# Kernel optimization log

Measured on AMD Instinct MI355X. Metric: run time of the kernel, lower is better.

The kernel has to match this reference:

```python
import jax, jax.numpy as jnp
import numpy as np

SEQ, BATCH, IN, HID, OUT = 512, 64, 64, 1024, 1


def _lstm_layer(x, W_ih, W_hh, b_ih, b_hh):
    # x: [T, B, I]; PyTorch gate order: i, f, g, o along 4H axis
    B = x.shape[1]
    H = W_hh.shape[1]
    xg = jnp.einsum('tbi,gi->tbg', x, W_ih) + b_ih + b_hh  # [T, B, 4H]

    def step(carry, xg_t):
        h, c = carry
        gates = xg_t + h @ W_hh.T  # [B, 4H]
        i, f, g, o = jnp.split(gates, 4, axis=-1)
        i = jax.nn.sigmoid(i)
        f = jax.nn.sigmoid(f)
        g = jnp.tanh(g)
        o = jax.nn.sigmoid(o)
        c = f * c + i * g
        h = o * jnp.tanh(c)
        return (h, c), h

    h0 = jnp.zeros((B, H), x.dtype)
    (_, _), hs = jax.lax.scan(step, (h0, h0), xg)
    return hs  # [T, B, H]


def setup_inputs() -> dict:
    key = jax.random.key(0)
    ks = jax.random.split(key, 12)
    s0 = 1.0 / np.sqrt(HID)
    d = {
        'x': jax.random.normal(ks[0], (SEQ, BATCH, IN), jnp.float32),
        'W_ih0': jax.random.uniform(ks[1], (4 * HID, IN), jnp.float32, -s0, s0),
        'W_hh0': jax.random.uniform(ks[2], (4 * HID, HID), jnp.float32, -s0, s0),
        'b_ih0': jax.random.uniform(ks[3], (4 * HID,), jnp.float32, -s0, s0),
        'b_hh0': jax.random.uniform(ks[4], (4 * HID,), jnp.float32, -s0, s0),
        'W_ih1': jax.random.uniform(ks[5], (4 * HID, HID), jnp.float32, -s0, s0),
        'W_hh1': jax.random.uniform(ks[6], (4 * HID, HID), jnp.float32, -s0, s0),
        'b_ih1': jax.random.uniform(ks[7], (4 * HID,), jnp.float32, -s0, s0),
        'b_hh1': jax.random.uniform(ks[8], (4 * HID,), jnp.float32, -s0, s0),
        'W_lin': jax.random.uniform(ks[9], (OUT, HID), jnp.float32, -s0, s0),
        'b_lin': jax.random.uniform(ks[10], (OUT,), jnp.float32, -s0, s0),
    }
    return d


def reference(x, W_ih0, W_hh0, b_ih0, b_hh0, W_ih1, W_hh1, b_ih1, b_hh1, W_lin, b_lin):
    h1 = _lstm_layer(x, W_ih0, W_hh0, b_ih0, b_hh0)   # [T, B, H]
    lstm_out = _lstm_layer(h1, W_ih1, W_hh1, b_ih1, b_hh1)  # [T, B, H]
    y_pred = lstm_out[-1] @ W_lin.T + b_lin           # [B, 1]
    return lstm_out, y_pred.reshape(-1)
```

## Files before the change

kernel.cpp:

```cpp
#include <hip/hip_runtime.h>
#include <stdint.h>

#define SEQ   512
#define BATCH 64
#define INP   64
#define HID   1024
#define NBLK  512
#define NTHR  256
#define CHK   32
#define NCH   (HID / CHK)
#define PRE   (CHK * 64 / NTHR)

__device__ __forceinline__ float cload(float* p) {
    return __hip_atomic_load(p, __ATOMIC_RELAXED, __HIP_MEMORY_SCOPE_AGENT);
}
__device__ __forceinline__ void cstore(float* p, float v) {
    __hip_atomic_store(p, v, __ATOMIC_RELAXED, __HIP_MEMORY_SCOPE_AGENT);
}

__device__ __forceinline__ float sigf(float x) { return 1.0f / (1.0f + __expf(-x)); }

__device__ __forceinline__ void flagbar(uint32_t* flags, int tid) {
    __syncthreads();
    if (tid == 0)
        __hip_atomic_store(&flags[blockIdx.x], 1u, __ATOMIC_RELAXED, __HIP_MEMORY_SCOPE_AGENT);
    if (tid < 64) {
        for (;;) {
            bool ok = true;
            #pragma unroll
            for (int i = 0; i < NBLK / 64; ++i) {
                uint32_t v = __hip_atomic_load(&flags[tid + i * 64], __ATOMIC_RELAXED,
                                               __HIP_MEMORY_SCOPE_AGENT);
                ok &= ((uint32_t)(v - 1u) < 0x10000000u);
            }
            if (__all(ok)) break;
        }
    }
    __syncthreads();
}

__device__ __forceinline__ void bar_arrive(uint32_t* grp, int tid) {
    __syncthreads();
    if (tid == 0)
        __hip_atomic_fetch_add(&grp[blockIdx.x & 7], 1u, __ATOMIC_RELAXED,
                               __HIP_MEMORY_SCOPE_AGENT);
}
__device__ __forceinline__ void bar_wait(uint32_t* grp, uint32_t target, int tid) {
    if (tid < 64) {
        for (;;) {
            uint32_t v = __hip_atomic_load(&grp[tid & 7], __ATOMIC_RELAXED,
                                           __HIP_MEMORY_SCOPE_AGENT);
            if (__all((uint32_t)(v - target) < 0x10000000u)) break;
        }
    }
    __syncthreads();
}

__global__ void __launch_bounds__(NTHR, 2) lstm_fused(
    const float* __restrict__ x,
    const float* __restrict__ Wih0, const float* __restrict__ Whh0,
    const float* __restrict__ bih0, const float* __restrict__ bhh0,
    const float* __restrict__ Wih1, const float* __restrict__ Whh1,
    const float* __restrict__ bih1, const float* __restrict__ bhh1,
    float* __restrict__ out, float* __restrict__ h0buf, float* __restrict__ h2buf,
    uint32_t* __restrict__ flags, uint32_t* __restrict__ grp)
{
    __shared__ float Wsh[4][HID][4];
    __shared__ float st1[CHK * 64];
    __shared__ float st2[CHK * 64];
    const int tid = threadIdx.x;
    const int bk  = blockIdx.x;
    const bool Lb = (bk >= NBLK / 2);
    const int ub  = (Lb ? bk - NBLK / 2 : bk) * 4;
    const int u   = tid >> 6;
    const int b   = tid & 63;
    const int j   = ub + u;
    const int js  = ub + __builtin_amdgcn_readfirstlane(u);

    const float* Whh = Lb ? Whh1 : Whh0;
    for (int idx = tid; idx < 4 * 4 * HID; idx += NTHR) {
        int uu = idx >> 12, g = (idx >> 10) & 3, k = idx & (HID - 1);
        Wsh[uu][k][g] = Whh[((size_t)(g * HID + ub + uu)) * HID + k];
    }
    const float* bi = Lb ? bih1 : bih0;
    const float* bh = Lb ? bhh1 : bhh0;
    const float bias0 = bi[0 * HID + j] + bh[0 * HID + j];
    const float bias1 = bi[1 * HID + j] + bh[1 * HID + j];
    const float bias2 = bi[2 * HID + j] + bh[2 * HID + j];
    const float bias3 = bi[3 * HID + j] + bh[3 * HID + j];

    cstore((Lb ? h2buf : h0buf) + j * 64 + b, 0.0f);
    if (bk < 8 && tid == 0) {
        __hip_atomic_store(&grp[bk], 0u, __ATOMIC_RELAXED, __HIP_MEMORY_SCOPE_AGENT);
        __threadfence();
    }
    float c = 0.0f;
    flagbar(flags, tid);

    if (!Lb) {
        const float4* wi0 = (const float4*)(Wih0 + (size_t)(0 * HID + js) * INP);
        const float4* wi1 = (const float4*)(Wih0 + (size_t)(1 * HID + js) * INP);
        const float4* wi2 = (const float4*)(Wih0 + (size_t)(2 * HID + js) * INP);
        const float4* wi3 = (const float4*)(Wih0 + (size_t)(3 * HID + js) * INP);
        float a0 = bias0, a1 = bias1, a2 = bias2, a3 = bias3;
        {
            const float4* xr = (const float4*)(x + (size_t)b * INP);
            #pragma unroll
            for (int k4 = 0; k4 < INP / 4; ++k4) {
                float4 xv = xr[k4];
                float4 u0 = wi0[k4], u1 = wi1[k4], u2 = wi2[k4], u3 = wi3[k4];
                a0 += u0.x * xv.x + u0.y * xv.y + u0.z * xv.z + u0.w * xv.w;
                a1 += u1.x * xv.x + u1.y * xv.y + u1.z * xv.z + u1.w * xv.w;
                a2 += u2.x * xv.x + u2.y * xv.y + u2.z * xv.z + u2.w * xv.w;
                a3 += u3.x * xv.x + u3.y * xv.y + u3.z * xv.z + u3.w * xv.w;
            }
        }
        for (int t = 0; t < SEQ; ++t) {
            float* hr = h0buf + (t & 1) * (HID * 64);
            float* hw = h0buf + ((t & 1) ^ 1) * (HID * 64);
            float pre[PRE];
            #pragma unroll
            for (int i = 0; i < PRE; ++i) pre[i] = cload(hr + i * NTHR + tid);
            for (int cc = 0; cc < NCH; ++cc) {
                __syncthreads();
                #pragma unroll
                for (int i = 0; i < PRE; ++i) st1[i * NTHR + tid] = pre[i];
                if (cc + 1 < NCH) {
                    float* src = hr + (cc + 1) * (CHK * 64);
                    #pragma unroll
                    for (int i = 0; i < PRE; ++i) pre[i] = cload(src + i * NTHR + tid);
                }
                __syncthreads();
                #pragma unroll
                for (int kk = 0; kk < CHK; ++kk) {
                    int k = cc * CHK + kk;
                    float  hv = st1[kk * 64 + b];
                    float4 w  = *(const float4*)&Wsh[u][k][0];
                    a0 += w.x * hv; a1 += w.y * hv; a2 += w.z * hv; a3 += w.w * hv;
                }
            }
            float ig = sigf(a0), fg = sigf(a1), gg = tanhf(a2), og = sigf(a3);
            c = fg * c + ig * gg;
            float h = og * tanhf(c);
            cstore(hw + j * 64 + b, h);
            bar_arrive(grp, tid);
            if (t + 1 < SEQ) {
                a0 = bias0; a1 = bias1; a2 = bias2; a3 = bias3;
                const float4* xr = (const float4*)(x + ((size_t)(t + 1) * BATCH + b) * INP);
                #pragma unroll
                for (int k4 = 0; k4 < INP / 4; ++k4) {
                    float4 xv = xr[k4];
                    float4 u0 = wi0[k4], u1 = wi1[k4], u2 = wi2[k4], u3 = wi3[k4];
                    a0 += u0.x * xv.x + u0.y * xv.y + u0.z * xv.z + u0.w * xv.w;
                    a1 += u1.x * xv.x + u1.y * xv.y + u1.z * xv.z + u1.w * xv.w;
                    a2 += u2.x * xv.x + u2.y * xv.y + u2.z * xv.z + u2.w * xv.w;
                    a3 += u3.x * xv.x + u3.y * xv.y + u3.z * xv.z + u3.w * xv.w;
                }
                bar_wait(grp, (uint32_t)(t + 1) * 64u, tid);
            }
        }
    } else {
        const float* wr0 = Wih1 + (size_t)(0 * HID + js) * HID;
        const float* wr1 = Wih1 + (size_t)(1 * HID + js) * HID;
        const float* wr2 = Wih1 + (size_t)(2 * HID + js) * HID;
        const float* wr3 = Wih1 + (size_t)(3 * HID + js) * HID;
        for (int t = 0; t < SEQ; ++t) {
            bar_arrive(grp, tid);
            bar_wait(grp, (uint32_t)(t + 1) * 64u, tid);
            float* h1r = h0buf + ((t & 1) ^ 1) * (HID * 64);
            float* h2r = h2buf + (t & 1) * (HID * 64);
            float* h2w = h2buf + ((t & 1) ^ 1) * (HID * 64);
            float a0 = bias0, a1 = bias1, a2 = bias2, a3 = bias3;
            float p1[PRE], p2[PRE];
            #pragma unroll
            for (int i = 0; i < PRE; ++i) p1[i] = cload(h1r + i * NTHR + tid);
            #pragma unroll
            for (int i = 0; i < PRE; ++i) p2[i] = cload(h2r + i * NTHR + tid);
            for (int cc = 0; cc < NCH; ++cc) {
                __syncthreads();
                #pragma unroll
                for (int i = 0; i < PRE; ++i) st1[i * NTHR + tid] = p1[i];
                #pragma unroll
                for (int i = 0; i < PRE; ++i) st2[i * NTHR + tid] = p2[i];
                if (cc + 1 < NCH) {
                    float* s1 = h1r + (cc + 1) * (CHK * 64);
                    float* s2 = h2r + (cc + 1) * (CHK * 64);
                    #pragma unroll
                    for (int i = 0; i < PRE; ++i) p1[i] = cload(s1 + i * NTHR + tid);
                    #pragma unroll
                    for (int i = 0; i < PRE; ++i) p2[i] = cload(s2 + i * NTHR + tid);
                }
                __syncthreads();
                #pragma unroll
                for (int kk = 0; kk < CHK; ++kk) {
                    int k = cc * CHK + kk;
                    float  x1 = st1[kk * 64 + b];
                    float  hv = st2[kk * 64 + b];
                    float4 wh = *(const float4*)&Wsh[u][k][0];
                    a0 += wh.x * hv + wr0[k] * x1;
                    a1 += wh.y * hv + wr1[k] * x1;
                    a2 += wh.z * hv + wr2[k] * x1;
                    a3 += wh.w * hv + wr3[k] * x1;
                }
            }
            float ig = sigf(a0), fg = sigf(a1), gg = tanhf(a2), og = sigf(a3);
            c = fg * c + ig * gg;
            float h = og * tanhf(c);
            cstore(h2w + j * 64 + b, h);
            out[((size_t)t * BATCH + b) * HID + j] = h;
        }
    }
}

__global__ void lstm_finalize(const float* __restrict__ Wlin, const float* __restrict__ blin,
                              float* __restrict__ out, float* __restrict__ h2buf)
{
    __shared__ float red[256];
    const int b = blockIdx.x, tid = threadIdx.x;
    float p = 0.0f;
    for (int k = tid; k < HID; k += 256) p += cload(h2buf + k * 64 + b) * Wlin[k];
    red[tid] = p;
    __syncthreads();
    for (int s = 128; s > 0; s >>= 1) {
        if (tid < s) red[tid] += red[tid + s];
        __syncthreads();
    }
    if (tid == 0) out[(size_t)SEQ * BATCH * HID + b] = blin[0] + red[0];
}

extern "C" void kernel_launch(void* const* d_in, const int* in_sizes, int n_in,
                              void* d_out, int out_size, void* d_ws, size_t ws_size,
                              hipStream_t stream) {
    const float* x     = (const float*)d_in[0];
    const float* Wih0  = (const float*)d_in[1];
    const float* Whh0  = (const float*)d_in[2];
    const float* bih0  = (const float*)d_in[3];
    const float* bhh0  = (const float*)d_in[4];
    const float* Wih1  = (const float*)d_in[5];
    const float* Whh1  = (const float*)d_in[6];
    const float* bih1  = (const float*)d_in[7];
    const float* bhh1  = (const float*)d_in[8];
    const float* Wlin  = (const float*)d_in[9];
    const float* blin  = (const float*)d_in[10];
    float* out = (float*)d_out;

    float* ws = (float*)d_ws;
    float* h0buf = ws;
    float* h2buf = ws + 2 * HID * BATCH;
    uint32_t* flags = (uint32_t*)(ws + 4 * HID * BATCH);
    uint32_t* grp   = flags + NBLK;

    lstm_fused<<<dim3(NBLK), dim3(NTHR), 0, stream>>>(
        x, Wih0, Whh0, bih0, bhh0, Wih1, Whh1, bih1, bhh1, out, h0buf, h2buf, flags, grp);
    lstm_finalize<<<dim3(BATCH), dim3(256), 0, stream>>>(Wlin, blin, out, h2buf);
}
```

Measured before the change: 45.01 ms.

## Double-buffer hidden-state chunk loads with inline-asm dwordx4 coherent loads

```diff
diff --git a/kernel.cpp b/kernel.cpp
--- a/kernel.cpp
+++ b/kernel.cpp
@@ -9,7 +9,15 @@
 #define NTHR  256
 #define CHK   32
 #define NCH   (HID / CHK)
-#define PRE   (CHK * 64 / NTHR)
+
+typedef float f4 __attribute__((ext_vector_type(4)));
+
+__device__ __forceinline__ void cload4(f4* dst, const float* p) {
+    asm volatile("global_load_dwordx4 %0, %1, off sc0 sc1"
+                 : "=&v"(*dst) : "v"(p) : "memory");
+}
+#define WAITVM(n) do { asm volatile("s_waitcnt vmcnt(" #n ")" ::: "memory"); \
+                       __builtin_amdgcn_sched_barrier(0); } while (0)
 
 __device__ __forceinline__ float cload(float* p) {
     return __hip_atomic_load(p, __ATOMIC_RELAXED, __HIP_MEMORY_SCOPE_AGENT);
@@ -118,22 +126,40 @@
         for (int t = 0; t < SEQ; ++t) {
             float* hr = h0buf + (t & 1) * (HID * 64);
             float* hw = h0buf + ((t & 1) ^ 1) * (HID * 64);
-            float pre[PRE];
-            #pragma unroll
-            for (int i = 0; i < PRE; ++i) pre[i] = cload(hr + i * NTHR + tid);
-            for (int cc = 0; cc < NCH; ++cc) {
-                __syncthreads();
-                #pragma unroll
-                for (int i = 0; i < PRE; ++i) st1[i * NTHR + tid] = pre[i];
-                if (cc + 1 < NCH) {
-                    float* src = hr + (cc + 1) * (CHK * 64);
-                    #pragma unroll
-                    for (int i = 0; i < PRE; ++i) pre[i] = cload(src + i * NTHR + tid);
+            f4 pA[2], pB[2];
+            cload4(&pA[0], hr + 0 * 2048 +    0 + tid * 4);
+            cload4(&pA[1], hr + 0 * 2048 + 1024 + tid * 4);
+            cload4(&pB[0], hr + 1 * 2048 +    0 + tid * 4);
+            cload4(&pB[1], hr + 1 * 2048 + 1024 + tid * 4);
+            for (int cc = 0; cc < NCH; cc += 2) {
+                __syncthreads();
+                WAITVM(2);
+                *(f4*)&st1[   0 + tid * 4] = pA[0];
+                *(f4*)&st1[1024 + tid * 4] = pA[1];
+                if (cc + 2 < NCH) {
+                    cload4(&pA[0], hr + (cc + 2) * 2048 +    0 + tid * 4);
+                    cload4(&pA[1], hr + (cc + 2) * 2048 + 1024 + tid * 4);
                 }
                 __syncthreads();
                 #pragma unroll
                 for (int kk = 0; kk < CHK; ++kk) {
                     int k = cc * CHK + kk;
+                    float  hv = st1[kk * 64 + b];
+                    float4 w  = *(const float4*)&Wsh[u][k][0];
+                    a0 += w.x * hv; a1 += w.y * hv; a2 += w.z * hv; a3 += w.w * hv;
+                }
+                __syncthreads();
+                if (cc + 2 < NCH) { WAITVM(2); } else { WAITVM(0); }
+                *(f4*)&st1[   0 + tid * 4] = pB[0];
+                *(f4*)&st1[1024 + tid * 4] = pB[1];
+                if (cc + 3 < NCH) {
+                    cload4(&pB[0], hr + (cc + 3) * 2048 +    0 + tid * 4);
+                    cload4(&pB[1], hr + (cc + 3) * 2048 + 1024 + tid * 4);
+                }
+                __syncthreads();
+                #pragma unroll
+                for (int kk = 0; kk < CHK; ++kk) {
+                    int k = (cc + 1) * CHK + kk;
                     float  hv = st1[kk * 64 + b];
                     float4 w  = *(const float4*)&Wsh[u][k][0];
                     a0 += w.x * hv; a1 += w.y * hv; a2 += w.z * hv; a3 += w.w * hv;
@@ -171,29 +197,52 @@
             float* h2r = h2buf + (t & 1) * (HID * 64);
             float* h2w = h2buf + ((t & 1) ^ 1) * (HID * 64);
             float a0 = bias0, a1 = bias1, a2 = bias2, a3 = bias3;
-            float p1[PRE], p2[PRE];
-            #pragma unroll
-            for (int i = 0; i < PRE; ++i) p1[i] = cload(h1r + i * NTHR + tid);
-            #pragma unroll
-            for (int i = 0; i < PRE; ++i) p2[i] = cload(h2r + i * NTHR + tid);
-            for (int cc = 0; cc < NCH; ++cc) {
-                __syncthreads();
-                #pragma unroll
-                for (int i = 0; i < PRE; ++i) st1[i * NTHR + tid] = p1[i];
-                #pragma unroll
-                for (int i = 0; i < PRE; ++i) st2[i * NTHR + tid] = p2[i];
-                if (cc + 1 < NCH) {
-                    float* s1 = h1r + (cc + 1) * (CHK * 64);
-                    float* s2 = h2r + (cc + 1) * (CHK * 64);
-                    #pragma unroll
-                    for (int i = 0; i < PRE; ++i) p1[i] = cload(s1 + i * NTHR + tid);
-                    #pragma unroll
-                    for (int i = 0; i < PRE; ++i) p2[i] = cload(s2 + i * NTHR + tid);
+            f4 p1A[2], p1B[2], p2A[2], p2B[2];
+            cload4(&p1A[0], h1r +    0 + tid * 4);  cload4(&p1A[1], h1r + 1024 + tid * 4);
+            cload4(&p2A[0], h2r +    0 + tid * 4);  cload4(&p2A[1], h2r + 1024 + tid * 4);
+            cload4(&p1B[0], h1r + 2048 + tid * 4);  cload4(&p1B[1], h1r + 3072 + tid * 4);
+            cload4(&p2B[0], h2r + 2048 + tid * 4);  cload4(&p2B[1], h2r + 3072 + tid * 4);
+            for (int cc = 0; cc < NCH; cc += 2) {
+                __syncthreads();
+                WAITVM(4);
+                *(f4*)&st1[   0 + tid * 4] = p1A[0];
+                *(f4*)&st1[1024 + tid * 4] = p1A[1];
+                *(f4*)&st2[   0 + tid * 4] = p2A[0];
+                *(f4*)&st2[1024 + tid * 4] = p2A[1];
+                if (cc + 2 < NCH) {
+                    const float* s1 = h1r + (cc + 2) * 2048;
+                    const float* s2 = h2r + (cc + 2) * 2048;
+                    cload4(&p1A[0], s1 +    0 + tid * 4);  cload4(&p1A[1], s1 + 1024 + tid * 4);
+                    cload4(&p2A[0], s2 +    0 + tid * 4);  cload4(&p2A[1], s2 + 1024 + tid * 4);
                 }
                 __syncthreads();
                 #pragma unroll
                 for (int kk = 0; kk < CHK; ++kk) {
                     int k = cc * CHK + kk;
+                    float  x1 = st1[kk * 64 + b];
+                    float  hv = st2[kk * 64 + b];
+                    float4 wh = *(const float4*)&Wsh[u][k][0];
+                    a0 += wh.x * hv + wr0[k] * x1;
+                    a1 += wh.y * hv + wr1[k] * x1;
+                    a2 += wh.z * hv + wr2[k] * x1;
+                    a3 += wh.w * hv + wr3[k] * x1;
+                }
+                __syncthreads();
+                if (cc + 2 < NCH) { WAITVM(4); } else { WAITVM(0); }
+                *(f4*)&st1[   0 + tid * 4] = p1B[0];
+                *(f4*)&st1[1024 + tid * 4] = p1B[1];
+                *(f4*)&st2[   0 + tid * 4] = p2B[0];
+                *(f4*)&st2[1024 + tid * 4] = p2B[1];
+                if (cc + 3 < NCH) {
+                    const float* s1 = h1r + (cc + 3) * 2048;
+                    const float* s2 = h2r + (cc + 3) * 2048;
+                    cload4(&p1B[0], s1 +    0 + tid * 4);  cload4(&p1B[1], s1 + 1024 + tid * 4);
+                    cload4(&p2B[0], s2 +    0 + tid * 4);  cload4(&p2B[1], s2 + 1024 + tid * 4);
+                }
+                __syncthreads();
+                #pragma unroll
+                for (int kk = 0; kk < CHK; ++kk) {
+                    int k = (cc + 1) * CHK + kk;
                     float  x1 = st1[kk * 64 + b];
                     float  hv = st2[kk * 64 + b];
                     float4 wh = *(const float4*)&Wsh[u][k][0];
```

Result: slower. 48.33 ms (+7.4%).

## Restructure persistent LSTM: 256 blocks of 8 units, k-interleaved h layout, double-buffered loads

Applied to the files above, without the earlier changes.

```diff
diff --git a/kernel.cpp b/kernel.cpp
--- a/kernel.cpp
+++ b/kernel.cpp
@@ -5,11 +5,28 @@
 #define BATCH 64
 #define INP   64
 #define HID   1024
-#define NBLK  512
-#define NTHR  256
+#define NBLK  256
+#define NTHR  512
+#define NU    8
 #define CHK   32
-#define NCH   (HID / CHK)
-#define PRE   (CHK * 64 / NTHR)
+#define KG    8
+#define NCH   32
+#define CHW   2048
+#define HBUF  65536
+
+typedef float f4 __attribute__((ext_vector_type(4)));
+
+__device__ __forceinline__ void cload4(f4* dst, const float* p) {
+    asm volatile("global_load_dwordx4 %0, %1, off sc0 sc1"
+                 : "=&v"(*dst) : "v"(p) : "memory");
+}
+#define WAITVM(n) do { asm volatile("s_waitcnt vmcnt(" #n ")" ::: "memory"); \
+                       __builtin_amdgcn_sched_barrier(0); } while (0)
+#define BARR  do { __builtin_amdgcn_sched_barrier(0); \
+                   asm volatile("s_waitcnt lgkmcnt(0)" ::: "memory"); \
+                   __builtin_amdgcn_sched_barrier(0); \
+                   __builtin_amdgcn_s_barrier(); \
+                   __builtin_amdgcn_sched_barrier(0); } while (0)
 
 __device__ __forceinline__ float cload(float* p) {
     return __hip_atomic_load(p, __ATOMIC_RELAXED, __HIP_MEMORY_SCOPE_AGENT);
@@ -17,7 +34,6 @@
 __device__ __forceinline__ void cstore(float* p, float v) {
     __hip_atomic_store(p, v, __ATOMIC_RELAXED, __HIP_MEMORY_SCOPE_AGENT);
 }
-
 __device__ __forceinline__ float sigf(float x) { return 1.0f / (1.0f + __expf(-x)); }
 
 __device__ __forceinline__ void flagbar(uint32_t* flags, int tid) {
@@ -56,40 +72,33 @@
     __syncthreads();
 }
 
+
 __global__ void __launch_bounds__(NTHR, 2) lstm_fused(
     const float* __restrict__ x,
     const float* __restrict__ Wih0, const float* __restrict__ Whh0,
     const float* __restrict__ bih0, const float* __restrict__ bhh0,
     const float* __restrict__ Wih1, const float* __restrict__ Whh1,
     const float* __restrict__ bih1, const float* __restrict__ bhh1,
-    float* __restrict__ out, float* __restrict__ h0buf, float* __restrict__ h2buf,
+    float* __restrict__ out, float* __restrict__ h1buf, float* __restrict__ h2buf,
     uint32_t* __restrict__ flags, uint32_t* __restrict__ grp)
 {
-    __shared__ float Wsh[4][HID][4];
-    __shared__ float st1[CHK * 64];
-    __shared__ float st2[CHK * 64];
+    __shared__ f4 st1[2][NTHR];
+    __shared__ f4 st2[2][NTHR];
     const int tid = threadIdx.x;
     const int bk  = blockIdx.x;
     const bool Lb = (bk >= NBLK / 2);
-    const int ub  = (Lb ? bk - NBLK / 2 : bk) * 4;
-    const int u   = tid >> 6;
+    const int ub  = (Lb ? bk - NBLK / 2 : bk) * NU;
     const int b   = tid & 63;
-    const int j   = ub + u;
-    const int js  = ub + __builtin_amdgcn_readfirstlane(u);
-
-    const float* Whh = Lb ? Whh1 : Whh0;
-    for (int idx = tid; idx < 4 * 4 * HID; idx += NTHR) {
-        int uu = idx >> 12, g = (idx >> 10) & 3, k = idx & (HID - 1);
-        Wsh[uu][k][g] = Whh[((size_t)(g * HID + ub + uu)) * HID + k];
-    }
+    const int js  = ub + __builtin_amdgcn_readfirstlane(tid >> 6);
+
     const float* bi = Lb ? bih1 : bih0;
     const float* bh = Lb ? bhh1 : bhh0;
-    const float bias0 = bi[0 * HID + j] + bh[0 * HID + j];
-    const float bias1 = bi[1 * HID + j] + bh[1 * HID + j];
-    const float bias2 = bi[2 * HID + j] + bh[2 * HID + j];
-    const float bias3 = bi[3 * HID + j] + bh[3 * HID + j];
-
-    cstore((Lb ? h2buf : h0buf) + j * 64 + b, 0.0f);
+    const float bias0 = bi[0 * HID + js] + bh[0 * HID + js];
+    const float bias1 = bi[1 * HID + js] + bh[1 * HID + js];
+    const float bias2 = bi[2 * HID + js] + bh[2 * HID + js];
+    const float bias3 = bi[3 * HID + js] + bh[3 * HID + js];
+
+    cstore((Lb ? h2buf : h1buf) + (js >> 2) * 256 + b * 4 + (js & 3), 0.0f);
     if (bk < 8 && tid == 0) {
         __hip_atomic_store(&grp[bk], 0u, __ATOMIC_RELAXED, __HIP_MEMORY_SCOPE_AGENT);
         __threadfence();
@@ -102,6 +111,10 @@
         const float4* wi1 = (const float4*)(Wih0 + (size_t)(1 * HID + js) * INP);
         const float4* wi2 = (const float4*)(Wih0 + (size_t)(2 * HID + js) * INP);
         const float4* wi3 = (const float4*)(Wih0 + (size_t)(3 * HID + js) * INP);
+        const float4* wh0 = (const float4*)(Whh0 + (size_t)(0 * HID + js) * HID);
+        const float4* wh1 = (const float4*)(Whh0 + (size_t)(1 * HID + js) * HID);
+        const float4* wh2 = (const float4*)(Whh0 + (size_t)(2 * HID + js) * HID);
+        const float4* wh3 = (const float4*)(Whh0 + (size_t)(3 * HID + js) * HID);
         float a0 = bias0, a1 = bias1, a2 = bias2, a3 = bias3;
         {
             const float4* xr = (const float4*)(x + (size_t)b * INP);
@@ -115,34 +128,46 @@
                 a3 += u3.x * xv.x + u3.y * xv.y + u3.z * xv.z + u3.w * xv.w;
             }
         }
+        #define CONSUME0(PAR, CB) do {                                          \
+            _Pragma("unroll")                                                   \
+            for (int kl = 0; kl < KG; ++kl) {                                   \
+                f4 hv = st1[PAR][kl * 64 + b];                                  \
+                int kg = (CB) + kl;                                             \
+                float4 w0 = wh0[kg], w1 = wh1[kg], w2 = wh2[kg], w3 = wh3[kg];  \
+                a0 += w0.x*hv.x + w0.y*hv.y + w0.z*hv.z + w0.w*hv.w;            \
+                a1 += w1.x*hv.x + w1.y*hv.y + w1.z*hv.z + w1.w*hv.w;            \
+                a2 += w2.x*hv.x + w2.y*hv.y + w2.z*hv.z + w2.w*hv.w;            \
+                a3 += w3.x*hv.x + w3.y*hv.y + w3.z*hv.z + w3.w*hv.w;            \
+            } } while (0)
         for (int t = 0; t < SEQ; ++t) {
-            float* hr = h0buf + (t & 1) * (HID * 64);
-            float* hw = h0buf + ((t & 1) ^ 1) * (HID * 64);
-            float pre[PRE];
-            #pragma unroll
-            for (int i = 0; i < PRE; ++i) pre[i] = cload(hr + i * NTHR + tid);
-            for (int cc = 0; cc < NCH; ++cc) {
-                __syncthreads();
-                #pragma unroll
-                for (int i = 0; i < PRE; ++i) st1[i * NTHR + tid] = pre[i];
-                if (cc + 1 < NCH) {
-                    float* src = hr + (cc + 1) * (CHK * 64);
-                    #pragma unroll
-                    for (int i = 0; i < PRE; ++i) pre[i] = cload(src + i * NTHR + tid);
+            float* hr = h1buf + (t & 1) * HBUF;
+            float* hw = h1buf + ((t & 1) ^ 1) * HBUF;
+            f4 bA, bB;
+            cload4(&bA, hr + tid * 4);
+            cload4(&bB, hr + CHW + tid * 4);
+            WAITVM(1);
+            st1[0][tid] = bA;
+            cload4(&bA, hr + 2 * CHW + tid * 4);
+            BARR;
+            #pragma unroll 1
+            for (int cc = 0; cc < NCH; cc += 2) {
+                if (cc + 2 < NCH) { WAITVM(1); } else { WAITVM(0); }
+                st1[1][tid] = bB;
+                if (cc + 3 < NCH) cload4(&bB, hr + (size_t)(cc + 3) * CHW + tid * 4);
+                CONSUME0(0, cc * KG);
+                BARR;
+                if (cc + 2 < NCH) {
+                    if (cc + 3 < NCH) { WAITVM(1); } else { WAITVM(0); }
+                    st1[0][tid] = bA;
+                    if (cc + 4 < NCH) cload4(&bA, hr + (size_t)(cc + 4) * CHW + tid * 4);
                 }
-                __syncthreads();
-                #pragma unroll
-                for (int kk = 0; kk < CHK; ++kk) {
-                    int k = cc * CHK + kk;
-                    float  hv = st1[kk * 64 + b];
-                    float4 w  = *(const float4*)&Wsh[u][k][0];
-                    a0 += w.x * hv; a1 += w.y * hv; a2 += w.z * hv; a3 += w.w * hv;
-                }
+                CONSUME0(1, (cc + 1) * KG);
+                BARR;
             }
             float ig = sigf(a0), fg = sigf(a1), gg = tanhf(a2), og = sigf(a3);
             c = fg * c + ig * gg;
             float h = og * tanhf(c);
-            cstore(hw + j * 64 + b, h);
+            cstore(hw + (js >> 2) * 256 + b * 4 + (js & 3), h);
             bar_arrive(grp, tid);
             if (t + 1 < SEQ) {
                 a0 = bias0; a1 = bias1; a2 = bias2; a3 = bias3;
@@ -156,69 +181,88 @@
                     a2 += u2.x * xv.x + u2.y * xv.y + u2.z * xv.z + u2.w * xv.w;
                     a3 += u3.x * xv.x + u3.y * xv.y + u3.z * xv.z + u3.w * xv.w;
                 }
-                bar_wait(grp, (uint32_t)(t + 1) * 64u, tid);
+                bar_wait(grp, (uint32_t)(t + 1) * 32u, tid);
             }
         }
     } else {
-        const float* wr0 = Wih1 + (size_t)(0 * HID + js) * HID;
-        const float* wr1 = Wih1 + (size_t)(1 * HID + js) * HID;
-        const float* wr2 = Wih1 + (size_t)(2 * HID + js) * HID;
-        const float* wr3 = Wih1 + (size_t)(3 * HID + js) * HID;
+        const float4* vi0 = (const float4*)(Wih1 + (size_t)(0 * HID + js) * HID);
+        const float4* vi1 = (const float4*)(Wih1 + (size_t)(1 * HID + js) * HID);
+        const float4* vi2 = (const float4*)(Wih1 + (size_t)(2 * HID + js) * HID);
+        const float4* vi3 = (const float4*)(Wih1 + (size_t)(3 * HID + js) * HID);
+        const float4* vh0 = (const float4*)(Whh1 + (size_t)(0 * HID + js) * HID);
+        const float4* vh1 = (const float4*)(Whh1 + (size_t)(1 * HID + js) * HID);
+        const float4* vh2 = (const float4*)(Whh1 + (size_t)(2 * HID + js) * HID);
+        const float4* vh3 = (const float4*)(Whh1 + (size_t)(3 * HID + js) * HID);
+        #define CONSUME1(PAR, CB) do {                                          \
+            _Pragma("unroll")                                                   \
+            for (int kl = 0; kl < KG; ++kl) {                                   \
+                f4 xv = st1[PAR][kl * 64 + b];                                  \
+                f4 hv = st2[PAR][kl * 64 + b];                                  \
+                int kg = (CB) + kl;                                             \
+                float4 i0 = vi0[kg], i1 = vi1[kg], i2 = vi2[kg], i3 = vi3[kg];  \
+                float4 h0 = vh0[kg], h1 = vh1[kg], h2 = vh2[kg], h3 = vh3[kg];  \
+                a0 += i0.x*xv.x + i0.y*xv.y + i0.z*xv.z + i0.w*xv.w             \
+                    + h0.x*hv.x + h0.y*hv.y + h0.z*hv.z + h0.w*hv.w;            \
+                a1 += i1.x*xv.x + i1.y*xv.y + i1.z*xv.z + i1.w*xv.w             \
+                    + h1.x*hv.x + h1.y*hv.y + h1.z*hv.z + h1.w*hv.w;            \
+                a2 += i2.x*xv.x + i2.y*xv.y + i2.z*xv.z + i2.w*xv.w             \
+                    + h2.x*hv.x + h2.y*hv.y + h2.z*hv.z + h2.w*hv.w;            \
+                a3 += i3.x*xv.x + i3.y*xv.y + i3.z*xv.z + i3.w*xv.w             \
+                    + h3.x*hv.x + h3.y*hv.y + h3.z*hv.z + h3.w*hv.w;            \
+            } } while (0)
         for (int t = 0; t < SEQ; ++t) {
             bar_arrive(grp, tid);
-            bar_wait(grp, (uint32_t)(t + 1) * 64u, tid);
-            float* h1r = h0buf + ((t & 1) ^ 1) * (HID * 64);
-            float* h2r = h2buf + (t & 1) * (HID * 64);
-            float* h2w = h2buf + ((t & 1) ^ 1) * (HID * 64);
+            bar_wait(grp, (uint32_t)(t + 1) * 32u, tid);
+            float* h1r = h1buf + ((t & 1) ^ 1) * HBUF;
+            float* h2r = h2buf + (t & 1) * HBUF;
+            float* h2w = h2buf + ((t & 1) ^ 1) * HBUF;
             float a0 = bias0, a1 = bias1, a2 = bias2, a3 = bias3;
-            float p1[PRE], p2[PRE];
-            #pragma unroll
-            for (int i = 0; i < PRE; ++i) p1[i] = cload(h1r + i * NTHR + tid);
-            #pragma unroll
-            for (int i = 0; i < PRE; ++i) p2[i] = cload(h2r + i * NTHR + tid);
-            for (int cc = 0; cc < NCH; ++cc) {
-                __syncthreads();
-                #pragma unroll
-                for (int i = 0; i < PRE; ++i) st1[i * NTHR + tid] = p1[i];
-                #pragma unroll
-                for (int i = 0; i < PRE; ++i) st2[i * NTHR + tid] = p2[i];
-                if (cc + 1 < NCH) {
-                    float* s1 = h1r + (cc + 1) * (CHK * 64);
-                    float* s2 = h2r + (cc + 1) * (CHK * 64);
-                    #pragma unroll
-                    for (int i = 0; i < PRE; ++i) p1[i] = cload(s1 + i * NTHR + tid);
-                    #pragma unroll
-                    for (int i = 0; i < PRE; ++i) p2[i] = cload(s2 + i * NTHR + tid);
+            f4 b1A, b1B, b2A, b2B;
+            cload4(&b1A, h1r + tid * 4);        cload4(&b2A, h2r + tid * 4);
+            cload4(&b1B, h1r + CHW + tid * 4);  cload4(&b2B, h2r + CHW + tid * 4);
+            WAITVM(2);
+            st1[0][tid] = b1A;  st2[0][tid] = b2A;
+            cload4(&b1A, h1r + 2 * CHW + tid * 4);
+            cload4(&b2A, h2r + 2 * CHW + tid * 4);
+            BARR;
+            #pragma unroll 1
+            for (int cc = 0; cc < NCH; cc += 2) {
+                if (cc + 2 < NCH) { WAITVM(2); } else { WAITVM(0); }
+                st1[1][tid] = b1B;  st2[1][tid] = b2B;
+                if (cc + 3 < NCH) {
+                    cload4(&b1B, h1r + (size_t)(cc + 3) * CHW + tid * 4);
+                    cload4(&b2B, h2r + (size_t)(cc + 3) * CHW + tid * 4);
                 }
-                __syncthreads();
-                #pragma unroll
-                for (int kk = 0; kk < CHK; ++kk) {
-                    int k = cc * CHK + kk;
-                    float  x1 = st1[kk * 64 + b];
-                    float  hv = st2[kk * 64 + b];
-                    float4 wh = *(const float4*)&Wsh[u][k][0];
-                    a0 += wh.x * hv + wr0[k] * x1;
-                    a1 += wh.y * hv + wr1[k] * x1;
-                    a2 += wh.z * hv + wr2[k] * x1;
-                    a3 += wh.w * hv + wr3[k] * x1;
+                CONSUME1(0, cc * KG);
+                BARR;
+                if (cc + 2 < NCH) {
+                    if (cc + 3 < NCH) { WAITVM(2); } else { WAITVM(0); }
+                    st1[0][tid] = b1A;  st2[0][tid] = b2A;
+                    if (cc + 4 < NCH) {
+                        cload4(&b1A, h1r + (size_t)(cc + 4) * CHW + tid * 4);
+                        cload4(&b2A, h2r + (size_t)(cc + 4) * CHW + tid * 4);
+                    }
                 }
+                CONSUME1(1, (cc + 1) * KG);
+                BARR;
             }
             float ig = sigf(a0), fg = sigf(a1), gg = tanhf(a2), og = sigf(a3);
             c = fg * c + ig * gg;
             float h = og * tanhf(c);
-            cstore(h2w + j * 64 + b, h);
-            out[((size_t)t * BATCH + b) * HID + j] = h;
+            cstore(h2w + (js >> 2) * 256 + b * 4 + (js & 3), h);
+            out[((size_t)t * BATCH + b) * HID + js] = h;
         }
     }
 }
 
 __global__ void lstm_finalize(const float* __restrict__ Wlin, const float* __restrict__ blin,
-                              float* __restrict__ out, float* __restrict__ h2buf)
+                              float* __restrict__ out)
 {
     __shared__ float red[256];
     const int b = blockIdx.x, tid = threadIdx.x;
+    const float* h2 = out + ((size_t)(SEQ - 1) * BATCH + b) * HID;
     float p = 0.0f;
-    for (int k = tid; k < HID; k += 256) p += cload(h2buf + k * 64 + b) * Wlin[k];
+    for (int k = tid; k < HID; k += 256) p += h2[k] * Wlin[k];
     red[tid] = p;
     __syncthreads();
     for (int s = 128; s > 0; s >>= 1) {
@@ -245,12 +289,12 @@
     float* out = (float*)d_out;
 
     float* ws = (float*)d_ws;
-    float* h0buf = ws;
-    float* h2buf = ws + 2 * HID * BATCH;
-    uint32_t* flags = (uint32_t*)(ws + 4 * HID * BATCH);
+    float* h1buf = ws;
+    float* h2buf = ws + 2 * HBUF;
+    uint32_t* flags = (uint32_t*)(ws + 4 * HBUF);
     uint32_t* grp   = flags + NBLK;
 
     lstm_fused<<<dim3(NBLK), dim3(NTHR), 0, stream>>>(
-        x, Wih0, Whh0, bih0, bhh0, Wih1, Whh1, bih1, bhh1, out, h0buf, h2buf, flags, grp);
-    lstm_finalize<<<dim3(BATCH), dim3(256), 0, stream>>>(Wlin, blin, out, h2buf);
-}
+        x, Wih0, Whh0, bih0, bhh0, Wih1, Whh1, bih1, bhh1, out, h1buf, h2buf, flags, grp);
+    lstm_finalize<<<dim3(BATCH), dim3(256), 0, stream>>>(Wlin, blin, out);
+}
```

Result: slower. 107.6 ms (+139.0%).
